# Kernel optimization log

Measured on AMD Instinct MI355X. Metric: run time of the kernel, lower is better.

## Reference

```python
import jax, jax.numpy as jnp
import numpy as np

BATCH = 4096
IN_DIM = 512
OUT_DIM = 512
GRID_SIZE = 5
K = 3


def _extended_grid():
    # Original: grid = linspace(-1, 1, grid_size+1), spacing h = 2/grid_size.
    # The de Boor-Cox recursion in the source indexes up to grid[grid_size+2k],
    # so we extend the uniform grid to the right with the same spacing.
    h = 2.0 / GRID_SIZE
    return (-1.0 + h * jnp.arange(GRID_SIZE + 2 * K + 1)).astype(jnp.float32)


def bspline_basis(x, grid, k):
    """Vectorized de Boor-Cox recursion.
    x: [..., ] floats; returns basis [..., grid_size + k].
    Identical math to the recursive b_spline_basis in the source, but computed
    bottom-up over all knot intervals at once (no redundant recomputation).
    """
    xe = x[..., None]  # [..., 1]
    # degree-0: indicator of half-open knot intervals, [..., n_knots-1]
    B = ((grid[:-1] <= xe) & (xe < grid[1:])).astype(x.dtype)
    for d in range(1, k + 1):
        n = grid.shape[0] - d - 1
        gi, gid = grid[:n], grid[d:d + n]          # grid[i], grid[i+d]
        gi1, gid1 = grid[1:n + 1], grid[d + 1:d + n + 1]  # grid[i+1], grid[i+d+1]
        # uniform grid -> denominators are d*h, never zero
        B = (xe - gi) / (gid - gi) * B[..., :n] + (gid1 - xe) / (gid1 - gi1) * B[..., 1:n + 1]
    return B  # [..., grid_size + k]


def setup_inputs() -> dict:
    key = jax.random.key(0)
    k1, k2 = jax.random.split(key)
    x = jax.random.uniform(k1, (BATCH, IN_DIM), jnp.float32) * 2.0 - 1.0  # in [-1, 1)
    spline_coeff = jax.random.normal(k2, (IN_DIM, OUT_DIM, GRID_SIZE + K), jnp.float32)
    spline_scaling = jnp.ones((IN_DIM, OUT_DIM), jnp.float32)
    return {"x": x, "spline_coeff": spline_coeff, "spline_scaling": spline_scaling}


def reference(x, spline_coeff, spline_scaling):
    grid = _extended_grid()
    basis = bspline_basis(x, grid, K)  # [B, in_dim, grid_size+k]
    # out[b, j] = sum_i scaling[i,j] * sum_g basis[b,i,g] * coeff[i,j,g]
    return jnp.einsum('big,ijg,ij->bj', basis, spline_coeff, spline_scaling)
```

## Files before the change

### kernel.cpp

```cpp
#include <hip/hip_runtime.h>
#include <hip/hip_bf16.h>
#include <stdint.h>


#define BATCH   4096
#define IN_DIM  512
#define OUT_DIM 512
#define KDIM    (IN_DIM * 8)

typedef short short8 __attribute__((ext_vector_type(8)));
typedef float f32x4  __attribute__((ext_vector_type(4)));

__device__ __forceinline__ unsigned short f2bf(float f) {
  union { float f; unsigned int u; } v; v.f = f;
  unsigned int r = v.u + 0x7FFFu + ((v.u >> 16) & 1u);
  return (unsigned short)(r >> 16);
}

__device__ __forceinline__ void bspline_win(float xv, float* w, int* mm) {
  float t = (xv + 1.0f) * 2.5f;
  int m = (int)t;
  m = m < 0 ? 0 : (m > 4 ? 4 : m);
  float u  = t - (float)m;
  float u2 = u * u, u3 = u2 * u, om = 1.0f - u;
  w[0] = om * om * om * (1.0f / 6.0f);
  w[1] = (3.0f * u3 - 6.0f * u2 + 4.0f) * (1.0f / 6.0f);
  w[2] = (-3.0f * u3 + 3.0f * u2 + 3.0f * u + 1.0f) * (1.0f / 6.0f);
  w[3] = u3 * (1.0f / 6.0f);
  *mm = m;
}

__device__ __forceinline__ short8 basis_pack8(float xv) {
  float w[4]; int m;
  bspline_win(xv, w, &m);
  short8 h = {};
#pragma unroll
  for (int g = 0; g < 8; ++g) {
    int d = g - m + 3;
    float v = (d == 0) ? w[0] : (d == 1) ? w[1] : (d == 2) ? w[2] : (d == 3) ? w[3] : 0.0f;
    h[g] = (short)f2bf(v);
  }
  return h;
}

__device__ __forceinline__ void async_load16(const void* g, void* l) {
  __builtin_amdgcn_global_load_lds(
      (__attribute__((address_space(1))) void*)(uintptr_t)g,
      (__attribute__((address_space(3))) void*)(unsigned int)(uintptr_t)l,
      16, 0, 0);
}

__global__ void kan_prep(const float* __restrict__ x,
                         const float* __restrict__ coeff,
                         const float* __restrict__ scaling,
                         unsigned short* __restrict__ Ag,
                         unsigned short* __restrict__ Wt) {
  const int b = blockIdx.x;
  if (b < (BATCH * IN_DIM) / 256) {
    int idx = b * 256 + threadIdx.x;
    short8 h = basis_pack8(x[idx]);
    *reinterpret_cast<short8*>(Ag + (size_t)idx * 8) = h;
  } else {
    int idx = (b - (BATCH * IN_DIM) / 256) * 256 + threadIdx.x;
    int i = idx >> 9, j = idx & 511;
    float s = scaling[idx];
    const float4* cp = reinterpret_cast<const float4*>(coeff) + (size_t)idx * 2;
    float4 c0 = cp[0], c1 = cp[1];
    short8 h;
    h[0] = (short)f2bf(c0.x * s); h[1] = (short)f2bf(c0.y * s);
    h[2] = (short)f2bf(c0.z * s); h[3] = (short)f2bf(c0.w * s);
    h[4] = (short)f2bf(c1.x * s); h[5] = (short)f2bf(c1.y * s);
    h[6] = (short)f2bf(c1.z * s); h[7] = (short)f2bf(c1.w * s);
    *reinterpret_cast<short8*>(Wt + (size_t)j * KDIM + i * 8) = h;
  }
}

__global__ __launch_bounds__(256, 2)
void kan_gemm_x(const unsigned short* __restrict__ Ag,
                const unsigned short* __restrict__ Wt,
                float* __restrict__ out) {
  __shared__ unsigned short As[64 * 64];
  __shared__ unsigned short Bs[64 * 64];

  const int tid  = threadIdx.x;
  const int lane = tid & 63;
  const int wid  = tid >> 6;
  const int wm = wid >> 1, wn = wid & 1;
  const int ln = lane & 15, quad = lane >> 4;

  const int b    = blockIdx.x;
  const int row0 = (b & 63) * 64;
  const int col0 = (b >> 6) * 64;

  f32x4 acc[2][2] = {};

  const int lr = lane >> 3;
  const int cg = (lane & 7) ^ lr;

  for (int kt = 0; kt < KDIM / 64; ++kt) {
    const int k0 = kt * 64;
#pragma unroll
    for (int t = 0; t < 2; ++t) {
      const int rbase = wid * 16 + t * 8;
      const unsigned short* ga = Ag + (size_t)(row0 + rbase + lr) * KDIM + k0 + cg * 8;
      async_load16(ga, &As[rbase * 64]);
      const unsigned short* gb = Wt + (size_t)(col0 + rbase + lr) * KDIM + k0 + cg * 8;
      async_load16(gb, &Bs[rbase * 64]);
    }
    __syncthreads();

#pragma unroll
    for (int kk = 0; kk < 2; ++kk) {
      short8 af[2], bfr[2];
#pragma unroll
      for (int mt = 0; mt < 2; ++mt) {
        const int r  = wm * 32 + mt * 16 + ln;
        const int pc = (kk * 4 + quad) ^ (r & 7);
        af[mt] = *reinterpret_cast<const short8*>(&As[r * 64 + pc * 8]);
      }
#pragma unroll
      for (int nt = 0; nt < 2; ++nt) {
        const int c  = wn * 32 + nt * 16 + ln;
        const int pc = (kk * 4 + quad) ^ (c & 7);
        bfr[nt] = *reinterpret_cast<const short8*>(&Bs[c * 64 + pc * 8]);
      }
#pragma unroll
      for (int mt = 0; mt < 2; ++mt)
#pragma unroll
        for (int nt = 0; nt < 2; ++nt)
          acc[mt][nt] = __builtin_amdgcn_mfma_f32_16x16x32_bf16(af[mt], bfr[nt], acc[mt][nt], 0, 0, 0);
    }
    __syncthreads();
  }

#pragma unroll
  for (int mt = 0; mt < 2; ++mt)
#pragma unroll
    for (int nt = 0; nt < 2; ++nt) {
      const int col = col0 + wn * 32 + nt * 16 + ln;
#pragma unroll
      for (int r = 0; r < 4; ++r) {
        const int row = row0 + wm * 32 + mt * 16 + quad * 4 + r;
        out[(size_t)row * OUT_DIM + col] = acc[mt][nt][r];
      }
    }
}

__global__ __launch_bounds__(256, 2)
void kan_gemm_fb(const float* __restrict__ x, const float* __restrict__ coeff,
                 const float* __restrict__ scaling, float* __restrict__ out) {
  __shared__ unsigned short As[64 * 64];
  __shared__ unsigned short Bs[64 * 64];

  const int tid  = threadIdx.x;
  const int lane = tid & 63;
  const int wid  = tid >> 6;
  const int wm = wid >> 1, wn = wid & 1;
  const int ln = lane & 15, quad = lane >> 4;
  const int row0 = blockIdx.y * 64;
  const int col0 = blockIdx.x * 64;

  f32x4 acc[2][2] = {};

  for (int kt = 0; kt < KDIM / 64; ++kt) {
#pragma unroll
    for (int pp = 0; pp < 2; ++pp) {
      const int p  = tid + pp * 256;
      const int rn = p & 63;
      const int il = p >> 6;
      const int sw = ((il ^ (rn & 7)) * 8);
      short8 ha = basis_pack8(x[(size_t)(row0 + rn) * IN_DIM + kt * 8 + il]);
      *reinterpret_cast<short8*>(&As[rn * 64 + sw]) = ha;
      const float* cbase = coeff + (size_t)(kt * 8 + il) * 4096 + (size_t)(col0 + rn) * 8;
      float4 c0 = reinterpret_cast<const float4*>(cbase)[0];
      float4 c1 = reinterpret_cast<const float4*>(cbase)[1];
      float s = scaling[(size_t)(kt * 8 + il) * OUT_DIM + col0 + rn];
      short8 hb;
      hb[0] = (short)f2bf(c0.x * s); hb[1] = (short)f2bf(c0.y * s);
      hb[2] = (short)f2bf(c0.z * s); hb[3] = (short)f2bf(c0.w * s);
      hb[4] = (short)f2bf(c1.x * s); hb[5] = (short)f2bf(c1.y * s);
      hb[6] = (short)f2bf(c1.z * s); hb[7] = (short)f2bf(c1.w * s);
      *reinterpret_cast<short8*>(&Bs[rn * 64 + sw]) = hb;
    }
    __syncthreads();
#pragma unroll
    for (int kk = 0; kk < 2; ++kk) {
      short8 af[2], bfr[2];
#pragma unroll
      for (int mt = 0; mt < 2; ++mt) {
        const int r  = wm * 32 + mt * 16 + ln;
        const int pc = (kk * 4 + quad) ^ (r & 7);
        af[mt] = *reinterpret_cast<const short8*>(&As[r * 64 + pc * 8]);
      }
#pragma unroll
      for (int nt = 0; nt < 2; ++nt) {
        const int c  = wn * 32 + nt * 16 + ln;
        const int pc = (kk * 4 + quad) ^ (c & 7);
        bfr[nt] = *reinterpret_cast<const short8*>(&Bs[c * 64 + pc * 8]);
      }
#pragma unroll
      for (int mt = 0; mt < 2; ++mt)
#pragma unroll
        for (int nt = 0; nt < 2; ++nt)
          acc[mt][nt] = __builtin_amdgcn_mfma_f32_16x16x32_bf16(af[mt], bfr[nt], acc[mt][nt], 0, 0, 0);
    }
    __syncthreads();
  }
#pragma unroll
  for (int mt = 0; mt < 2; ++mt)
#pragma unroll
    for (int nt = 0; nt < 2; ++nt) {
      const int col = col0 + wn * 32 + nt * 16 + ln;
#pragma unroll
      for (int r = 0; r < 4; ++r) {
        const int row = row0 + wm * 32 + mt * 16 + quad * 4 + r;
        out[(size_t)row * OUT_DIM + col] = acc[mt][nt][r];
      }
    }
}

extern "C" void kernel_launch(void* const* d_in, const int* in_sizes, int n_in,
                              void* d_out, int out_size, void* d_ws, size_t ws_size,
                              hipStream_t stream) {
  const float* x       = (const float*)d_in[0];
  const float* coeff   = (const float*)d_in[1];
  const float* scaling = (const float*)d_in[2];
  float* out = (float*)d_out;

  const size_t needA = (size_t)BATCH * KDIM * 2;
  const size_t needW = (size_t)OUT_DIM * KDIM * 2;

  if (ws_size >= needA + needW) {
    unsigned short* Ag = (unsigned short*)d_ws;
    unsigned short* Wt = (unsigned short*)((char*)d_ws + needA);
    kan_prep<<<(BATCH * IN_DIM) / 256 + (IN_DIM * OUT_DIM) / 256, 256, 0, stream>>>(
        x, coeff, scaling, Ag, Wt);
    kan_gemm_x<<<(BATCH / 64) * (OUT_DIM / 64), 256, 0, stream>>>(Ag, Wt, out);
  } else {
    kan_gemm_fb<<<dim3(OUT_DIM / 64, BATCH / 64), 256, 0, stream>>>(x, coeff, scaling, out);
  }
}
```

Before: 113.9 us.

## Triple-buffer async LDS loads in GEMM with vmcnt-based waits

Turns the single-buffered GEMM main loop into a three-stage software pipeline. Global-to-LDS async loads are issued three K-tiles ahead, and explicit s_waitcnt vmcnt values plus raw barriers replace the full __syncthreads drain on every iteration. This is meant to hide global memory latency behind MFMA work. It triples LDS use to 48KB per block, which may limit occupancy, and it relies on hand-coded waitcnt encodings being correct.

```diff
diff --git a/kernel.cpp b/kernel.cpp
--- a/kernel.cpp
+++ b/kernel.cpp
@@ -7,9 +7,14 @@
 #define IN_DIM  512
 #define OUT_DIM 512
 #define KDIM    (IN_DIM * 8)
+#define NKT     (KDIM / 64)
 
 typedef short short8 __attribute__((ext_vector_type(8)));
 typedef float f32x4  __attribute__((ext_vector_type(4)));
+
+#define WAIT_VM8 0xF78
+#define WAIT_VM4 0xF74
+#define WAIT_VM0 0xF70
 
 __device__ __forceinline__ unsigned short f2bf(float f) {
   union { float f; unsigned int u; } v; v.f = f;
@@ -76,11 +81,11 @@
 }
 
 __global__ __launch_bounds__(256, 2)
-void kan_gemm_x(const unsigned short* __restrict__ Ag,
+void kan_gemm_p(const unsigned short* __restrict__ Ag,
                 const unsigned short* __restrict__ Wt,
                 float* __restrict__ out) {
-  __shared__ unsigned short As[64 * 64];
-  __shared__ unsigned short Bs[64 * 64];
+  __shared__ unsigned short As[3][64 * 64];
+  __shared__ unsigned short Bs[3][64 * 64];
 
   const int tid  = threadIdx.x;
   const int lane = tid & 63;
@@ -97,32 +102,34 @@
   const int lr = lane >> 3;
   const int cg = (lane & 7) ^ lr;
 
-  for (int kt = 0; kt < KDIM / 64; ++kt) {
+  const unsigned short* aRow = Ag + (size_t)(row0 + wid * 16 + lr) * KDIM + cg * 8;
+  const unsigned short* bRow = Wt + (size_t)(col0 + wid * 16 + lr) * KDIM + cg * 8;
+
+  auto issue = [&](int kt, int st) {
     const int k0 = kt * 64;
 #pragma unroll
     for (int t = 0; t < 2; ++t) {
       const int rbase = wid * 16 + t * 8;
-      const unsigned short* ga = Ag + (size_t)(row0 + rbase + lr) * KDIM + k0 + cg * 8;
-      async_load16(ga, &As[rbase * 64]);
-      const unsigned short* gb = Wt + (size_t)(col0 + rbase + lr) * KDIM + k0 + cg * 8;
-      async_load16(gb, &Bs[rbase * 64]);
-    }
-    __syncthreads();
-
+      async_load16(aRow + (size_t)t * 8 * KDIM + k0, &As[st][rbase * 64]);
+      async_load16(bRow + (size_t)t * 8 * KDIM + k0, &Bs[st][rbase * 64]);
+    }
+  };
+
+  auto compute = [&](int st) {
 #pragma unroll
     for (int kk = 0; kk < 2; ++kk) {
       short8 af[2], bfr[2];
 #pragma unroll
       for (int mt = 0; mt < 2; ++mt) {
-        const int r  = wm * 32 + mt * 16 + ln;
-        const int pc = (kk * 4 + quad) ^ (r & 7);
-        af[mt] = *reinterpret_cast<const short8*>(&As[r * 64 + pc * 8]);
+        const int r    = wm * 32 + mt * 16 + ln;
+        const int slot = (kk * 4 + quad) ^ (r & 7);
+        af[mt] = *reinterpret_cast<const short8*>(&As[st][r * 64 + slot * 8]);
       }
 #pragma unroll
       for (int nt = 0; nt < 2; ++nt) {
-        const int c  = wn * 32 + nt * 16 + ln;
-        const int pc = (kk * 4 + quad) ^ (c & 7);
-        bfr[nt] = *reinterpret_cast<const short8*>(&Bs[c * 64 + pc * 8]);
+        const int c    = wn * 32 + nt * 16 + ln;
+        const int slot = (kk * 4 + quad) ^ (c & 7);
+        bfr[nt] = *reinterpret_cast<const short8*>(&Bs[st][c * 64 + slot * 8]);
       }
 #pragma unroll
       for (int mt = 0; mt < 2; ++mt)
@@ -130,8 +137,30 @@
         for (int nt = 0; nt < 2; ++nt)
           acc[mt][nt] = __builtin_amdgcn_mfma_f32_16x16x32_bf16(af[mt], bfr[nt], acc[mt][nt], 0, 0, 0);
     }
-    __syncthreads();
-  }
+  };
+
+  issue(0, 0); issue(1, 1); issue(2, 2);
+
+  int st = 0;
+  for (int kt = 0; kt < NKT - 3; ++kt) {
+    __builtin_amdgcn_s_waitcnt(WAIT_VM8);
+    __builtin_amdgcn_s_barrier();
+    compute(st);
+    __builtin_amdgcn_s_barrier();
+    issue(kt + 3, st);
+    st = (st == 2) ? 0 : st + 1;
+  }
+  __builtin_amdgcn_s_waitcnt(WAIT_VM8);
+  __builtin_amdgcn_s_barrier();
+  compute(st);
+  st = (st == 2) ? 0 : st + 1;
+  __builtin_amdgcn_s_waitcnt(WAIT_VM4);
+  __builtin_amdgcn_s_barrier();
+  compute(st);
+  st = (st == 2) ? 0 : st + 1;
+  __builtin_amdgcn_s_waitcnt(WAIT_VM0);
+  __builtin_amdgcn_s_barrier();
+  compute(st);
 
 #pragma unroll
   for (int mt = 0; mt < 2; ++mt)
@@ -235,7 +264,7 @@
     unsigned short* Wt = (unsigned short*)((char*)d_ws + needA);
     kan_prep<<<(BATCH * IN_DIM) / 256 + (IN_DIM * OUT_DIM) / 256, 256, 0, stream>>>(
         x, coeff, scaling, Ag, Wt);
-    kan_gemm_x<<<(BATCH / 64) * (OUT_DIM / 64), 256, 0, stream>>>(Ag, Wt, out);
+    kan_gemm_p<<<(BATCH / 64) * (OUT_DIM / 64), 256, 0, stream>>>(Ag, Wt, out);
   } else {
     kan_gemm_fb<<<dim3(OUT_DIM / 64, BATCH / 64), 256, 0, stream>>>(x, coeff, scaling, out);
   }
```

After: 98.75 us. -13.3%, faster.
